# Performance work log

Hardware: AMD Instinct MI355X
Metric: run time of the kernel (lower is better)

The kernel has to match this reference:

```python
import jax, jax.numpy as jnp
import numpy as np
import math


def setup_inputs() -> dict:
    key = jax.random.key(0)
    k1, k2, k3 = jax.random.split(key, 3)
    shape = (2, 16, 2048, 64)  # (b, h, s, d)
    Q = jax.random.normal(k1, shape, dtype=jnp.float32)
    K = jax.random.normal(k2, shape, dtype=jnp.float32)
    V = jax.random.normal(k3, shape, dtype=jnp.float32)
    return {"Q": Q, "K": K, "V": V}


def reference(Q, K, V):
    b, h, s, d = Q.shape
    scale = jnp.float16(1.0 / math.sqrt(d))
    # Faithful to the torch module: fp16 QK^T and PV matmuls, fp32 softmax.
    Qh = Q.astype(jnp.float16)
    Kh = K.astype(jnp.float16)
    Vh = V.astype(jnp.float16)
    # [b,h,s,s] scores in fp16 (materialized, as in the original baddbmm)
    scores = jnp.einsum('bhsd,bhtd->bhst', Qh, Kh) * scale
    attn = jax.nn.softmax(scores.astype(jnp.float32), axis=-1).astype(jnp.float16)
    out = jnp.einsum('bhst,bhtd->bhsd', attn, Vh)
    return out.astype(jnp.float32)
```

## Files before the change

kernel.cpp:

```cpp
#include <hip/hip_runtime.h>
#include <stdint.h>

typedef _Float16 half8 __attribute__((ext_vector_type(8)));
typedef _Float16 half4 __attribute__((ext_vector_type(4)));
typedef __fp16 fp16x2 __attribute__((ext_vector_type(2)));
typedef float f32x4 __attribute__((ext_vector_type(4)));
typedef float float4v __attribute__((ext_vector_type(4)));

#define S_LEN 2048
#define D_DIM 64
#define QBLK 128
#define KVBLK 64
#define NT (S_LEN / KVBLK)
#define NBH 32
#define QSCALE 0.18033688f
#define KSTR 72

#if __has_builtin(__builtin_amdgcn_exp2f)
#define EXP2(x) __builtin_amdgcn_exp2f(x)
#else
#define EXP2(x) exp2f(x)
#endif
#define MAX3(a, b, c) fmaxf(fmaxf((a), (b)), (c))

static __device__ __forceinline__ void glds16(const void* g, void* l) {
  __builtin_amdgcn_global_load_lds(
      (__attribute__((address_space(1))) void*)(g),
      (__attribute__((address_space(3))) void*)(l), 16, 0, 0);
}
#define SBAR() do { asm volatile("" ::: "memory"); __builtin_amdgcn_s_barrier(); asm volatile("" ::: "memory"); } while (0)

__global__ __launch_bounds__(256)
void cvt_pack(const float* __restrict__ Kg, const float* __restrict__ Vg,
              _Float16* __restrict__ Kw, _Float16* __restrict__ Vw) {
  const int id = (int)(blockIdx.x * 256 + threadIdx.x);
  const int tensor = id >> 19;
  const int cid = id & 0x7FFFF;
  const int bht = cid >> 9;
  const int bh = bht >> 5, t = bht & 31;
  const int loc = cid & 511;
  const int a = loc >> 3;
  const int s = loc & 7;
  size_t srcoff;
  if (tensor == 0) {
    const int r = a;
    srcoff = (size_t)bh * (S_LEN * D_DIM) + (size_t)(t * 64 + r) * D_DIM + 8 * (s ^ (r & 7));
  } else {
    const int TI = a, c2 = s;
    const int it = TI & 3;
    const int vgi = ((TI >> 3) & 3) | (((TI >> 2) & 1) << 2) | (((TI >> 5) & 1) << 3);
    const int kq = c2 >> 1, d8 = (c2 & 1) * 8;
    srcoff = (size_t)bh * (S_LEN * D_DIM) + (size_t)(t * 64 + 4 * vgi + kq) * D_DIM + it * 16 + d8;
  }
  const float* src = (tensor ? Vg : Kg) + srcoff;
  float4v x = *(const float4v*)src;
  float4v y = *(const float4v*)(src + 4);
  half8 h = { (_Float16)x[0], (_Float16)x[1], (_Float16)x[2], (_Float16)x[3],
              (_Float16)y[0], (_Float16)y[1], (_Float16)y[2], (_Float16)y[3] };
  _Float16* dst = (tensor ? Vw : Kw) + (size_t)bht * 4096 + (size_t)loc * 8;
  *(half8*)dst = h;
}

static __device__ __forceinline__ void softmax_pack(f32x4 (&s)[4], float& m_run,
                                                    f32x4& l_acc, f32x4 (&o)[4],
                                                    half8 (&pb)[2]) {
  float plm;
  {
    float a0 = MAX3(s[0][0], s[0][1], s[0][2]);
    float a1 = MAX3(s[0][3], s[1][0], s[1][1]);
    float a2 = MAX3(s[1][2], s[1][3], s[2][0]);
    float a3 = MAX3(s[2][1], s[2][2], s[2][3]);
    float a4 = MAX3(s[3][0], s[3][1], s[3][2]);
    plm = fmaxf(MAX3(a0, a1, a2), MAX3(a3, a4, s[3][3]));
  }
  float p[16];
  if (__any(plm > m_run + 8.f)) {
    float pmax = fmaxf(plm, __shfl_xor(plm, 16, 64));
    pmax = fmaxf(pmax, __shfl_xor(pmax, 32, 64));
    const float mnew  = fmaxf(m_run, pmax);
    const float alpha = EXP2(m_run - mnew);
    m_run = mnew;
#pragma unroll
    for (int i = 0; i < 16; ++i)
      p[i] = EXP2(s[i >> 2][i & 3] - mnew);
    l_acc[0] *= alpha;
#pragma unroll
    for (int dt = 0; dt < 4; ++dt) {
      o[dt][0] *= alpha; o[dt][1] *= alpha;
      o[dt][2] *= alpha; o[dt][3] *= alpha;
    }
  } else {
#pragma unroll
    for (int i = 0; i < 16; ++i)
      p[i] = EXP2(s[i >> 2][i & 3] - m_run);
  }
#pragma unroll
  for (int kc = 0; kc < 2; ++kc) {
    fp16x2 x0 = __builtin_amdgcn_cvt_pkrtz(p[8 * kc + 0], p[8 * kc + 1]);
    fp16x2 x1 = __builtin_amdgcn_cvt_pkrtz(p[8 * kc + 2], p[8 * kc + 3]);
    fp16x2 x2 = __builtin_amdgcn_cvt_pkrtz(p[8 * kc + 4], p[8 * kc + 5]);
    fp16x2 x3 = __builtin_amdgcn_cvt_pkrtz(p[8 * kc + 6], p[8 * kc + 7]);
    half8 pk = { (_Float16)x0[0], (_Float16)x0[1], (_Float16)x1[0], (_Float16)x1[1],
                 (_Float16)x2[0], (_Float16)x2[1], (_Float16)x3[0], (_Float16)x3[1] };
    pb[kc] = pk;
  }
}

__global__ __launch_bounds__(256, 2)
void fa_fwd2(const float* __restrict__ Qg, const _Float16* __restrict__ Kw,
             const _Float16* __restrict__ Vw, float* __restrict__ Og) {
  __shared__ __attribute__((aligned(128))) _Float16 Klds[4][4096];
  __shared__ __attribute__((aligned(128))) _Float16 Vlds[4][4096];

  const int tid  = (int)threadIdx.x;
  const int wid  = tid >> 6;
  const int lane = tid & 63;
  const int g    = lane >> 4;
  const int c    = lane & 15;

  const int qtile = (int)blockIdx.x;
  const int bh    = (int)blockIdx.y;
  const size_t base = (size_t)bh * (S_LEN * D_DIM);

  const int qrowA = qtile * QBLK + wid * 16 + c;
  const int qrowB = qrowA + 64;
  half8 qfA[2], qfB[2];
#pragma unroll
  for (int kt = 0; kt < 2; ++kt) {
    const float* qpA = Qg + base + (size_t)qrowA * D_DIM + kt * 32 + 8 * g;
    const float* qpB = Qg + base + (size_t)qrowB * D_DIM + kt * 32 + 8 * g;
    float4v a0 = *(const float4v*)qpA;
    float4v a1 = *(const float4v*)(qpA + 4);
    float4v b0 = *(const float4v*)qpB;
    float4v b1 = *(const float4v*)(qpB + 4);
    half8 qa = { (_Float16)(a0[0] * QSCALE), (_Float16)(a0[1] * QSCALE),
                 (_Float16)(a0[2] * QSCALE), (_Float16)(a0[3] * QSCALE),
                 (_Float16)(a1[0] * QSCALE), (_Float16)(a1[1] * QSCALE),
                 (_Float16)(a1[2] * QSCALE), (_Float16)(a1[3] * QSCALE) };
    half8 qb = { (_Float16)(b0[0] * QSCALE), (_Float16)(b0[1] * QSCALE),
                 (_Float16)(b0[2] * QSCALE), (_Float16)(b0[3] * QSCALE),
                 (_Float16)(b1[0] * QSCALE), (_Float16)(b1[1] * QSCALE),
                 (_Float16)(b1[2] * QSCALE), (_Float16)(b1[3] * QSCALE) };
    qfA[kt] = qa; qfB[kt] = qb;
  }

  const f32x4 zero4 = {0.f, 0.f, 0.f, 0.f};
  f32x4 o_accA[4], o_accB[4];
#pragma unroll
  for (int i = 0; i < 4; ++i) { o_accA[i] = zero4; o_accB[i] = zero4; }
  f32x4 l_accA = zero4, l_accB = zero4;
  const half8 ones8 = { (_Float16)1.f, (_Float16)1.f, (_Float16)1.f, (_Float16)1.f,
                        (_Float16)1.f, (_Float16)1.f, (_Float16)1.f, (_Float16)1.f };
  float m_runA = -1.0e30f, m_runB = -1.0e30f;

  const char* kbase = (const char*)Kw + ((size_t)(bh * NT) << 13);
  const char* vbase = (const char*)Vw + ((size_t)(bh * NT) << 13);
  const int woff = wid * 2048 + lane * 16;

#define STAGE(b, t) do { \
    const char* ks_ = kbase + ((size_t)(t) << 13) + woff; \
    const char* vs_ = vbase + ((size_t)(t) << 13) + woff; \
    glds16(ks_,        &Klds[(b)][wid * 1024]); \
    glds16(ks_ + 1024, &Klds[(b)][wid * 1024 + 512]); \
    glds16(vs_,        &Vlds[(b)][wid * 1024]); \
    glds16(vs_ + 1024, &Vlds[(b)][wid * 1024 + 512]); \
  } while (0)

  const uint32_t vtb0 = (uint32_t)(uintptr_t)(&Vlds[0][0]) + 1024u * (uint32_t)g + 8u * (uint32_t)c;

  asm volatile("s_waitcnt vmcnt(0)" ::: "memory");
  STAGE(0, 0);
  STAGE(1, 1);

  for (int t = 0; t < NT; ++t) {
    if (t + 2 < NT) {
      STAGE((t + 2) & 3, t + 2);
      asm volatile("s_waitcnt vmcnt(8)" ::: "memory");
    } else if (t + 1 < NT) {
      asm volatile("s_waitcnt vmcnt(4)" ::: "memory");
    } else {
      asm volatile("s_waitcnt vmcnt(0)" ::: "memory");
    }
    __builtin_amdgcn_sched_barrier(0);
    SBAR();

    const _Float16* kcur = &Klds[t & 3][0];
    const uint32_t vt = vtb0 + (uint32_t)((t & 3) << 13);

    f32x4 sA[4], sB[4];
#pragma unroll
    for (int ct = 0; ct < 4; ++ct) { sA[ct] = zero4; sB[ct] = zero4; }
    __builtin_amdgcn_s_setprio(1);
#pragma unroll
    for (int ct = 0; ct < 4; ++ct) {
#pragma unroll
      for (int kt = 0; kt < 2; ++kt) {
        half8 kb = *(half8*)&kcur[(ct * 16 + c) * 64 + (((4 * kt + g) ^ (c & 7)) << 3)];
        sA[ct] = __builtin_amdgcn_mfma_f32_16x16x32_f16(kb, qfA[kt], sA[ct], 0, 0, 0);
        sB[ct] = __builtin_amdgcn_mfma_f32_16x16x32_f16(kb, qfB[kt], sB[ct], 0, 0, 0);
      }
    }
    __builtin_amdgcn_s_setprio(0);

    half4 vr[16];
#define TRRD(i, offstr) \
    asm volatile("ds_read_b64_tr_b16 %0, %1 offset:" offstr : "=v"(vr[i]) : "v"(vt))
    TRRD(0,  "0");    TRRD(1,  "128");  TRRD(2,  "256");  TRRD(3,  "384");
    TRRD(4,  "512");  TRRD(5,  "640");  TRRD(6,  "768");  TRRD(7,  "896");
    TRRD(8,  "4096"); TRRD(9,  "4224"); TRRD(10, "4352"); TRRD(11, "4480");
    TRRD(12, "4608"); TRRD(13, "4736"); TRRD(14, "4864"); TRRD(15, "4992");
#undef TRRD

    half8 pbA[2], pbB[2];
    softmax_pack(sA, m_runA, l_accA, o_accA, pbA);
    softmax_pack(sB, m_runB, l_accB, o_accB, pbB);

    asm volatile("s_waitcnt lgkmcnt(0)" ::: "memory");
    __builtin_amdgcn_sched_barrier(0);

    __builtin_amdgcn_s_setprio(1);
#pragma unroll
    for (int kc = 0; kc < 2; ++kc) {
#pragma unroll
      for (int dt = 0; dt < 4; ++dt) {
        half8 vf = __builtin_shufflevector(vr[kc * 8 + dt], vr[kc * 8 + 4 + dt],
                                           0, 1, 2, 3, 4, 5, 6, 7);
        o_accA[dt] = __builtin_amdgcn_mfma_f32_16x16x32_f16(vf, pbA[kc], o_accA[dt], 0, 0, 0);
        o_accB[dt] = __builtin_amdgcn_mfma_f32_16x16x32_f16(vf, pbB[kc], o_accB[dt], 0, 0, 0);
      }
      l_accA = __builtin_amdgcn_mfma_f32_16x16x32_f16(ones8, pbA[kc], l_accA, 0, 0, 0);
      l_accB = __builtin_amdgcn_mfma_f32_16x16x32_f16(ones8, pbB[kc], l_accB, 0, 0, 0);
    }
    __builtin_amdgcn_s_setprio(0);
  }
#undef STAGE

  const float invA = 1.0f / l_accA[0];
  const float invB = 1.0f / l_accB[0];
#pragma unroll
  for (int dt = 0; dt < 4; ++dt) {
    float4v wA = { o_accA[dt][0] * invA, o_accA[dt][1] * invA,
                   o_accA[dt][2] * invA, o_accA[dt][3] * invA };
    *(float4v*)&Og[base + (size_t)qrowA * D_DIM + dt * 16 + g * 4] = wA;
    float4v wB = { o_accB[dt][0] * invB, o_accB[dt][1] * invB,
                   o_accB[dt][2] * invB, o_accB[dt][3] * invB };
    *(float4v*)&Og[base + (size_t)qrowB * D_DIM + dt * 16 + g * 4] = wB;
  }
}

__global__ __launch_bounds__(256)
void fa_fwd_fb(const float* __restrict__ Qg, const float* __restrict__ Kg,
               const float* __restrict__ Vg, float* __restrict__ Og) {
  __shared__ _Float16 Klds[KVBLK * KSTR];
  __shared__ __attribute__((aligned(128))) _Float16 Vlds[KVBLK * D_DIM];

  const int tid  = (int)threadIdx.x;
  const int wid  = tid >> 6;
  const int lane = tid & 63;
  const int g    = lane >> 4;
  const int c    = lane & 15;

  const int qtile = (int)blockIdx.x;
  const int bh    = (int)blockIdx.y;
  const size_t base = (size_t)bh * (S_LEN * D_DIM);

  const int qrow = qtile * 64 + wid * 16 + c;
  half8 qf[2];
#pragma unroll
  for (int kt = 0; kt < 2; ++kt) {
    const float* qp = Qg + base + (size_t)qrow * D_DIM + kt * 32 + 8 * g;
    float4v a = *(const float4v*)qp;
    float4v b = *(const float4v*)(qp + 4);
    half8 q;
    q[0] = (_Float16)(a[0] * QSCALE); q[1] = (_Float16)(a[1] * QSCALE);
    q[2] = (_Float16)(a[2] * QSCALE); q[3] = (_Float16)(a[3] * QSCALE);
    q[4] = (_Float16)(b[0] * QSCALE); q[5] = (_Float16)(b[1] * QSCALE);
    q[6] = (_Float16)(b[2] * QSCALE); q[7] = (_Float16)(b[3] * QSCALE);
    qf[kt] = q;
  }

  const f32x4 zero4 = {0.f, 0.f, 0.f, 0.f};
  f32x4 o_acc[4];
#pragma unroll
  for (int i = 0; i < 4; ++i) o_acc[i] = zero4;
  float m_run = -1.0e30f, l_run = 0.f;

  const int srow = tid >> 4;
  const int scol = (tid & 15) * 4;
  const int vgi = tid >> 4;
  const int vlg = tid & 15;
  const int vk  = vgi * 4 + (vlg >> 2);
  const int vsub = 8 * (vgi & 3) + 4 * ((vgi >> 2) & 1) + 32 * (vgi >> 3);
  const uint32_t vtb = (uint32_t)(uintptr_t)(&Vlds[0]) + 1024u * (uint32_t)g + 8u * (uint32_t)c;

  for (int t = 0; t < NT; ++t) {
    const int kv0 = t * KVBLK;
    __syncthreads();
#pragma unroll
    for (int rr = 0; rr < 4; ++rr) {
      const int row = srow + rr * 16;
      const float* kp = Kg + base + (size_t)(kv0 + row) * D_DIM + scol;
      float4v kx = *(const float4v*)kp;
      half4 kh = { (_Float16)kx[0], (_Float16)kx[1], (_Float16)kx[2], (_Float16)kx[3] };
      *(half4*)&Klds[row * KSTR + scol] = kh;
    }
#pragma unroll
    for (int it = 0; it < 4; ++it) {
      const int d = it * 16 + (vlg & 3) * 4;
      const float* vp = Vg + base + (size_t)(kv0 + vk) * D_DIM + d;
      float4v vx = *(const float4v*)vp;
      half4 vh = { (_Float16)vx[0], (_Float16)vx[1], (_Float16)vx[2], (_Float16)vx[3] };
      *(half4*)&Vlds[(vsub + it) * 64 + (vlg >> 2) * 16 + (vlg & 3) * 4] = vh;
    }
    __syncthreads();

    f32x4 s_acc[4];
#pragma unroll
    for (int ct = 0; ct < 4; ++ct) s_acc[ct] = zero4;
#pragma unroll
    for (int ct = 0; ct < 4; ++ct) {
#pragma unroll
      for (int kt = 0; kt < 2; ++kt) {
        half8 kb = *(half8*)&Klds[(ct * 16 + c) * KSTR + kt * 32 + 8 * g];
        s_acc[ct] = __builtin_amdgcn_mfma_f32_16x16x32_f16(kb, qf[kt], s_acc[ct], 0, 0, 0);
      }
    }

    float pmax = -1.0e30f;
#pragma unroll
    for (int ct = 0; ct < 4; ++ct)
#pragma unroll
      for (int r = 0; r < 4; ++r) pmax = fmaxf(pmax, s_acc[ct][r]);
    pmax = fmaxf(pmax, __shfl_xor(pmax, 16, 64));
    pmax = fmaxf(pmax, __shfl_xor(pmax, 32, 64));
    const float mnew  = fmaxf(m_run, pmax);
    const float alpha = exp2f(m_run - mnew);
    m_run = mnew;

    float p[16];
    float psum = 0.f;
#pragma unroll
    for (int i = 0; i < 16; ++i) {
      p[i] = exp2f(s_acc[i >> 2][i & 3] - mnew);
      psum += p[i];
    }
    psum += __shfl_xor(psum, 16, 64);
    psum += __shfl_xor(psum, 32, 64);
    l_run = l_run * alpha + psum;
#pragma unroll
    for (int dt = 0; dt < 4; ++dt) {
      o_acc[dt][0] *= alpha; o_acc[dt][1] *= alpha;
      o_acc[dt][2] *= alpha; o_acc[dt][3] *= alpha;
    }

    half8 pb[2];
#pragma unroll
    for (int kc = 0; kc < 2; ++kc) {
      fp16x2 x0 = __builtin_amdgcn_cvt_pkrtz(p[8 * kc + 0], p[8 * kc + 1]);
      fp16x2 x1 = __builtin_amdgcn_cvt_pkrtz(p[8 * kc + 2], p[8 * kc + 3]);
      fp16x2 x2 = __builtin_amdgcn_cvt_pkrtz(p[8 * kc + 4], p[8 * kc + 5]);
      fp16x2 x3 = __builtin_amdgcn_cvt_pkrtz(p[8 * kc + 6], p[8 * kc + 7]);
      half8 pk = { (_Float16)x0[0], (_Float16)x0[1], (_Float16)x1[0], (_Float16)x1[1],
                   (_Float16)x2[0], (_Float16)x2[1], (_Float16)x3[0], (_Float16)x3[1] };
      pb[kc] = pk;
    }

    half4 vr[16];
#define TRRD(i, offstr) \
    asm volatile("ds_read_b64_tr_b16 %0, %1 offset:" offstr : "=v"(vr[i]) : "v"(vtb))
    TRRD(0,  "0");    TRRD(1,  "128");  TRRD(2,  "256");  TRRD(3,  "384");
    TRRD(4,  "512");  TRRD(5,  "640");  TRRD(6,  "768");  TRRD(7,  "896");
    TRRD(8,  "4096"); TRRD(9,  "4224"); TRRD(10, "4352"); TRRD(11, "4480");
    TRRD(12, "4608"); TRRD(13, "4736"); TRRD(14, "4864"); TRRD(15, "4992");
#undef TRRD
    asm volatile("s_waitcnt lgkmcnt(0)" ::: "memory");
    __builtin_amdgcn_sched_barrier(0);

#pragma unroll
    for (int kc = 0; kc < 2; ++kc) {
#pragma unroll
      for (int dt = 0; dt < 4; ++dt) {
        half8 vf = __builtin_shufflevector(vr[kc * 8 + dt], vr[kc * 8 + 4 + dt],
                                           0, 1, 2, 3, 4, 5, 6, 7);
        o_acc[dt] = __builtin_amdgcn_mfma_f32_16x16x32_f16(vf, pb[kc], o_acc[dt], 0, 0, 0);
      }
    }
  }

  const float invl = 1.0f / l_run;
#pragma unroll
  for (int dt = 0; dt < 4; ++dt) {
    float4v w = { o_acc[dt][0] * invl, o_acc[dt][1] * invl,
                  o_acc[dt][2] * invl, o_acc[dt][3] * invl };
    *(float4v*)&Og[base + (size_t)qrow * D_DIM + dt * 16 + g * 4] = w;
  }
}

extern "C" void kernel_launch(void* const* d_in, const int* in_sizes, int n_in,
                              void* d_out, int out_size, void* d_ws, size_t ws_size,
                              hipStream_t stream) {
  const float* Q = (const float*)d_in[0];
  const float* K = (const float*)d_in[1];
  const float* V = (const float*)d_in[2];
  float* O = (float*)d_out;
  dim3 block(256);
  if (ws_size >= (size_t)16 * 1024 * 1024) {
    _Float16* Kw = (_Float16*)d_ws;
    _Float16* Vw = Kw + (size_t)NBH * S_LEN * D_DIM;
    hipLaunchKernelGGL(cvt_pack, dim3(4096), block, 0, stream, K, V, Kw, Vw);
    hipLaunchKernelGGL(fa_fwd2, dim3(S_LEN / QBLK, NBH), block, 0, stream, Q, Kw, Vw, O);
  } else {
    hipLaunchKernelGGL(fa_fwd_fb, dim3(S_LEN / 64, NBH), block, 0, stream, Q, K, V, O);
  }
}
```

Measured before the change: 62.97 us.

## Use 16x16x16 MFMA for PV and deepen K/V prefetch to three tiles

Splits each P·V and row-sum MFMA into two 16x16x16 f16 MFMAs fed directly from the transposed LDS reads, avoiding the half8 shuffles. It also prefetches three KV tiles ahead, issued after the barrier into the buffer freed in the previous iteration. The split doubles the MFMA instruction count, and the x16 variant may have lower throughput than x32 on this chip.

```diff
diff --git a/kernel.cpp b/kernel.cpp
--- a/kernel.cpp
+++ b/kernel.cpp
@@ -22,6 +22,12 @@
 #define EXP2(x) exp2f(x)
 #endif
 #define MAX3(a, b, c) fmaxf(fmaxf((a), (b)), (c))
+
+#if __has_builtin(__builtin_amdgcn_mfma_f32_16x16x16f16)
+#define HAVE_MFMA16 1
+#else
+#define HAVE_MFMA16 0
+#endif
 
 static __device__ __forceinline__ void glds16(const void* g, void* l) {
   __builtin_amdgcn_global_load_lds(
@@ -61,9 +67,9 @@
   *(half8*)dst = h;
 }
 
-static __device__ __forceinline__ void softmax_pack(f32x4 (&s)[4], float& m_run,
-                                                    f32x4& l_acc, f32x4 (&o)[4],
-                                                    half8 (&pb)[2]) {
+static __device__ __forceinline__ void softmax_pack16(f32x4 (&s)[4], float& m_run,
+                                                      f32x4& l_acc, f32x4 (&o)[4],
+                                                      half4 (&pb)[2][2]) {
   float plm;
   {
     float a0 = MAX3(s[0][0], s[0][1], s[0][2]);
@@ -100,9 +106,10 @@
     fp16x2 x1 = __builtin_amdgcn_cvt_pkrtz(p[8 * kc + 2], p[8 * kc + 3]);
     fp16x2 x2 = __builtin_amdgcn_cvt_pkrtz(p[8 * kc + 4], p[8 * kc + 5]);
     fp16x2 x3 = __builtin_amdgcn_cvt_pkrtz(p[8 * kc + 6], p[8 * kc + 7]);
-    half8 pk = { (_Float16)x0[0], (_Float16)x0[1], (_Float16)x1[0], (_Float16)x1[1],
-                 (_Float16)x2[0], (_Float16)x2[1], (_Float16)x3[0], (_Float16)x3[1] };
-    pb[kc] = pk;
+    half4 lo = { (_Float16)x0[0], (_Float16)x0[1], (_Float16)x1[0], (_Float16)x1[1] };
+    half4 hi = { (_Float16)x2[0], (_Float16)x2[1], (_Float16)x3[0], (_Float16)x3[1] };
+    pb[kc][0] = lo;
+    pb[kc][1] = hi;
   }
 }
 
@@ -149,9 +156,13 @@
 #pragma unroll
   for (int i = 0; i < 4; ++i) { o_accA[i] = zero4; o_accB[i] = zero4; }
   f32x4 l_accA = zero4, l_accB = zero4;
+  float m_runA = -1.0e30f, m_runB = -1.0e30f;
+#if HAVE_MFMA16
+  const half4 ones4 = { (_Float16)1.f, (_Float16)1.f, (_Float16)1.f, (_Float16)1.f };
+#else
   const half8 ones8 = { (_Float16)1.f, (_Float16)1.f, (_Float16)1.f, (_Float16)1.f,
                         (_Float16)1.f, (_Float16)1.f, (_Float16)1.f, (_Float16)1.f };
-  float m_runA = -1.0e30f, m_runB = -1.0e30f;
+#endif
 
   const char* kbase = (const char*)Kw + ((size_t)(bh * NT) << 13);
   const char* vbase = (const char*)Vw + ((size_t)(bh * NT) << 13);
@@ -171,18 +182,19 @@
   asm volatile("s_waitcnt vmcnt(0)" ::: "memory");
   STAGE(0, 0);
   STAGE(1, 1);
+  STAGE(2, 2);
 
   for (int t = 0; t < NT; ++t) {
-    if (t + 2 < NT) {
-      STAGE((t + 2) & 3, t + 2);
+    if (t <= NT - 3) {
       asm volatile("s_waitcnt vmcnt(8)" ::: "memory");
-    } else if (t + 1 < NT) {
+    } else if (t == NT - 2) {
       asm volatile("s_waitcnt vmcnt(4)" ::: "memory");
     } else {
       asm volatile("s_waitcnt vmcnt(0)" ::: "memory");
     }
     __builtin_amdgcn_sched_barrier(0);
     SBAR();
+    if (t + 3 < NT) STAGE((t + 3) & 3, t + 3);
 
     const _Float16* kcur = &Klds[t & 3][0];
     const uint32_t vt = vtb0 + (uint32_t)((t & 3) << 13);
@@ -211,26 +223,46 @@
     TRRD(12, "4608"); TRRD(13, "4736"); TRRD(14, "4864"); TRRD(15, "4992");
 #undef TRRD
 
-    half8 pbA[2], pbB[2];
-    softmax_pack(sA, m_runA, l_accA, o_accA, pbA);
-    softmax_pack(sB, m_runB, l_accB, o_accB, pbB);
+    half4 pbA[2][2], pbB[2][2];
+    softmax_pack16(sA, m_runA, l_accA, o_accA, pbA);
+    softmax_pack16(sB, m_runB, l_accB, o_accB, pbB);
 
     asm volatile("s_waitcnt lgkmcnt(0)" ::: "memory");
     __builtin_amdgcn_sched_barrier(0);
 
     __builtin_amdgcn_s_setprio(1);
+#if HAVE_MFMA16
+#pragma unroll
+    for (int kc = 0; kc < 2; ++kc) {
+#pragma unroll
+      for (int h = 0; h < 2; ++h) {
+#pragma unroll
+        for (int dt = 0; dt < 4; ++dt) {
+          o_accA[dt] = __builtin_amdgcn_mfma_f32_16x16x16f16(vr[kc * 8 + h * 4 + dt], pbA[kc][h], o_accA[dt], 0, 0, 0);
+          o_accB[dt] = __builtin_amdgcn_mfma_f32_16x16x16f16(vr[kc * 8 + h * 4 + dt], pbB[kc][h], o_accB[dt], 0, 0, 0);
+        }
+        l_accA = __builtin_amdgcn_mfma_f32_16x16x16f16(ones4, pbA[kc][h], l_accA, 0, 0, 0);
+        l_accB = __builtin_amdgcn_mfma_f32_16x16x16f16(ones4, pbB[kc][h], l_accB, 0, 0, 0);
+      }
+    }
+#else
 #pragma unroll
     for (int kc = 0; kc < 2; ++kc) {
 #pragma unroll
       for (int dt = 0; dt < 4; ++dt) {
         half8 vf = __builtin_shufflevector(vr[kc * 8 + dt], vr[kc * 8 + 4 + dt],
                                            0, 1, 2, 3, 4, 5, 6, 7);
-        o_accA[dt] = __builtin_amdgcn_mfma_f32_16x16x32_f16(vf, pbA[kc], o_accA[dt], 0, 0, 0);
-        o_accB[dt] = __builtin_amdgcn_mfma_f32_16x16x32_f16(vf, pbB[kc], o_accB[dt], 0, 0, 0);
+        half8 pA = __builtin_shufflevector(pbA[kc][0], pbA[kc][1], 0, 1, 2, 3, 4, 5, 6, 7);
+        half8 pB = __builtin_shufflevector(pbB[kc][0], pbB[kc][1], 0, 1, 2, 3, 4, 5, 6, 7);
+        o_accA[dt] = __builtin_amdgcn_mfma_f32_16x16x32_f16(vf, pA, o_accA[dt], 0, 0, 0);
+        o_accB[dt] = __builtin_amdgcn_mfma_f32_16x16x32_f16(vf, pB, o_accB[dt], 0, 0, 0);
       }
-      l_accA = __builtin_amdgcn_mfma_f32_16x16x32_f16(ones8, pbA[kc], l_accA, 0, 0, 0);
-      l_accB = __builtin_amdgcn_mfma_f32_16x16x32_f16(ones8, pbB[kc], l_accB, 0, 0, 0);
-    }
+      half8 pA = __builtin_shufflevector(pbA[kc][0], pbA[kc][1], 0, 1, 2, 3, 4, 5, 6, 7);
+      half8 pB = __builtin_shufflevector(pbB[kc][0], pbB[kc][1], 0, 1, 2, 3, 4, 5, 6, 7);
+      l_accA = __builtin_amdgcn_mfma_f32_16x16x32_f16(ones8, pA, l_accA, 0, 0, 0);
+      l_accB = __builtin_amdgcn_mfma_f32_16x16x32_f16(ones8, pB, l_accB, 0, 0, 0);
+    }
+#endif
     __builtin_amdgcn_s_setprio(0);
   }
 #undef STAGE
```

New measurement: 70.37 us. +11.7%, slower.

## Software-pipeline PV matmul of previous tile with QK and softmax of current

Applied to the files above, without the earlier changes.

Restructures the attention main loop so the P·V MFMA block for tile t-1 runs after the QK^T MFMAs and V transpose-reads of tile t, and before tile t's softmax. Double-buffered V-fragment and P registers alternate across an unrolled-by-two loop, with a prologue and an epilogue PV. The goal is to hide LDS transpose-read latency and the softmax VALU work behind matrix-core work. The cost is extra live VGPRs for the second V and P buffers, which could lower occupancy or cause spills.

```diff
diff --git a/kernel.cpp b/kernel.cpp
--- a/kernel.cpp
+++ b/kernel.cpp
@@ -168,71 +168,98 @@
 
   const uint32_t vtb0 = (uint32_t)(uintptr_t)(&Vlds[0][0]) + 1024u * (uint32_t)g + 8u * (uint32_t)c;
 
+  half4 vr0[16], vr1[16];
+  half8 pbA0[2], pbB0[2], pbA1[2], pbB1[2];
+
+#define TRRD_SET(VR, vt) do { \
+    asm volatile("ds_read_b64_tr_b16 %0, %1 offset:0"    : "=v"(VR[0])  : "v"(vt)); \
+    asm volatile("ds_read_b64_tr_b16 %0, %1 offset:128"  : "=v"(VR[1])  : "v"(vt)); \
+    asm volatile("ds_read_b64_tr_b16 %0, %1 offset:256"  : "=v"(VR[2])  : "v"(vt)); \
+    asm volatile("ds_read_b64_tr_b16 %0, %1 offset:384"  : "=v"(VR[3])  : "v"(vt)); \
+    asm volatile("ds_read_b64_tr_b16 %0, %1 offset:512"  : "=v"(VR[4])  : "v"(vt)); \
+    asm volatile("ds_read_b64_tr_b16 %0, %1 offset:640"  : "=v"(VR[5])  : "v"(vt)); \
+    asm volatile("ds_read_b64_tr_b16 %0, %1 offset:768"  : "=v"(VR[6])  : "v"(vt)); \
+    asm volatile("ds_read_b64_tr_b16 %0, %1 offset:896"  : "=v"(VR[7])  : "v"(vt)); \
+    asm volatile("ds_read_b64_tr_b16 %0, %1 offset:4096" : "=v"(VR[8])  : "v"(vt)); \
+    asm volatile("ds_read_b64_tr_b16 %0, %1 offset:4224" : "=v"(VR[9])  : "v"(vt)); \
+    asm volatile("ds_read_b64_tr_b16 %0, %1 offset:4352" : "=v"(VR[10]) : "v"(vt)); \
+    asm volatile("ds_read_b64_tr_b16 %0, %1 offset:4480" : "=v"(VR[11]) : "v"(vt)); \
+    asm volatile("ds_read_b64_tr_b16 %0, %1 offset:4608" : "=v"(VR[12]) : "v"(vt)); \
+    asm volatile("ds_read_b64_tr_b16 %0, %1 offset:4736" : "=v"(VR[13]) : "v"(vt)); \
+    asm volatile("ds_read_b64_tr_b16 %0, %1 offset:4864" : "=v"(VR[14]) : "v"(vt)); \
+    asm volatile("ds_read_b64_tr_b16 %0, %1 offset:4992" : "=v"(VR[15]) : "v"(vt)); \
+  } while (0)
+
+#define PV_BLOCK(VR, PBA, PBB) do { \
+    __builtin_amdgcn_s_setprio(1); \
+    _Pragma("unroll") \
+    for (int kc = 0; kc < 2; ++kc) { \
+      _Pragma("unroll") \
+      for (int dt = 0; dt < 4; ++dt) { \
+        half8 vf = __builtin_shufflevector(VR[kc * 8 + dt], VR[kc * 8 + 4 + dt], \
+                                           0, 1, 2, 3, 4, 5, 6, 7); \
+        o_accA[dt] = __builtin_amdgcn_mfma_f32_16x16x32_f16(vf, PBA[kc], o_accA[dt], 0, 0, 0); \
+        o_accB[dt] = __builtin_amdgcn_mfma_f32_16x16x32_f16(vf, PBB[kc], o_accB[dt], 0, 0, 0); \
+      } \
+      l_accA = __builtin_amdgcn_mfma_f32_16x16x32_f16(ones8, PBA[kc], l_accA, 0, 0, 0); \
+      l_accB = __builtin_amdgcn_mfma_f32_16x16x32_f16(ones8, PBB[kc], l_accB, 0, 0, 0); \
+    } \
+    __builtin_amdgcn_s_setprio(0); \
+  } while (0)
+
+#define ITER(T, VRC, PBAC, PBBC, DO_PV, VRP, PBAP, PBBP) do { \
+    if ((T) + 2 < NT) { \
+      STAGE(((T) + 2) & 3, (T) + 2); \
+      asm volatile("s_waitcnt vmcnt(8)" ::: "memory"); \
+    } else if ((T) + 1 < NT) { \
+      asm volatile("s_waitcnt vmcnt(4)" ::: "memory"); \
+    } else { \
+      asm volatile("s_waitcnt vmcnt(0)" ::: "memory"); \
+    } \
+    __builtin_amdgcn_sched_barrier(0); \
+    SBAR(); \
+    const _Float16* kcur = &Klds[(T) & 3][0]; \
+    const uint32_t vt = vtb0 + (uint32_t)(((T) & 3) << 13); \
+    f32x4 sA[4], sB[4]; \
+    _Pragma("unroll") \
+    for (int ct = 0; ct < 4; ++ct) { sA[ct] = zero4; sB[ct] = zero4; } \
+    __builtin_amdgcn_s_setprio(1); \
+    _Pragma("unroll") \
+    for (int ct = 0; ct < 4; ++ct) { \
+      _Pragma("unroll") \
+      for (int kt = 0; kt < 2; ++kt) { \
+        half8 kb = *(half8*)&kcur[(ct * 16 + c) * 64 + (((4 * kt + g) ^ (c & 7)) << 3)]; \
+        sA[ct] = __builtin_amdgcn_mfma_f32_16x16x32_f16(kb, qfA[kt], sA[ct], 0, 0, 0); \
+        sB[ct] = __builtin_amdgcn_mfma_f32_16x16x32_f16(kb, qfB[kt], sB[ct], 0, 0, 0); \
+      } \
+    } \
+    __builtin_amdgcn_s_setprio(0); \
+    TRRD_SET(VRC, vt); \
+    if (DO_PV) { \
+      asm volatile("s_waitcnt lgkmcnt(15)" ::: "memory");  \
+      __builtin_amdgcn_sched_barrier(0); \
+      PV_BLOCK(VRP, PBAP, PBBP); \
+    } \
+    softmax_pack(sA, m_runA, l_accA, o_accA, PBAC); \
+    softmax_pack(sB, m_runB, l_accB, o_accB, PBBC); \
+  } while (0)
+
   asm volatile("s_waitcnt vmcnt(0)" ::: "memory");
   STAGE(0, 0);
   STAGE(1, 1);
 
-  for (int t = 0; t < NT; ++t) {
-    if (t + 2 < NT) {
-      STAGE((t + 2) & 3, t + 2);
-      asm volatile("s_waitcnt vmcnt(8)" ::: "memory");
-    } else if (t + 1 < NT) {
-      asm volatile("s_waitcnt vmcnt(4)" ::: "memory");
-    } else {
-      asm volatile("s_waitcnt vmcnt(0)" ::: "memory");
-    }
-    __builtin_amdgcn_sched_barrier(0);
-    SBAR();
-
-    const _Float16* kcur = &Klds[t & 3][0];
-    const uint32_t vt = vtb0 + (uint32_t)((t & 3) << 13);
-
-    f32x4 sA[4], sB[4];
-#pragma unroll
-    for (int ct = 0; ct < 4; ++ct) { sA[ct] = zero4; sB[ct] = zero4; }
-    __builtin_amdgcn_s_setprio(1);
-#pragma unroll
-    for (int ct = 0; ct < 4; ++ct) {
-#pragma unroll
-      for (int kt = 0; kt < 2; ++kt) {
-        half8 kb = *(half8*)&kcur[(ct * 16 + c) * 64 + (((4 * kt + g) ^ (c & 7)) << 3)];
-        sA[ct] = __builtin_amdgcn_mfma_f32_16x16x32_f16(kb, qfA[kt], sA[ct], 0, 0, 0);
-        sB[ct] = __builtin_amdgcn_mfma_f32_16x16x32_f16(kb, qfB[kt], sB[ct], 0, 0, 0);
-      }
-    }
-    __builtin_amdgcn_s_setprio(0);
-
-    half4 vr[16];
-#define TRRD(i, offstr) \
-    asm volatile("ds_read_b64_tr_b16 %0, %1 offset:" offstr : "=v"(vr[i]) : "v"(vt))
-    TRRD(0,  "0");    TRRD(1,  "128");  TRRD(2,  "256");  TRRD(3,  "384");
-    TRRD(4,  "512");  TRRD(5,  "640");  TRRD(6,  "768");  TRRD(7,  "896");
-    TRRD(8,  "4096"); TRRD(9,  "4224"); TRRD(10, "4352"); TRRD(11, "4480");
-    TRRD(12, "4608"); TRRD(13, "4736"); TRRD(14, "4864"); TRRD(15, "4992");
-#undef TRRD
-
-    half8 pbA[2], pbB[2];
-    softmax_pack(sA, m_runA, l_accA, o_accA, pbA);
-    softmax_pack(sB, m_runB, l_accB, o_accB, pbB);
-
-    asm volatile("s_waitcnt lgkmcnt(0)" ::: "memory");
-    __builtin_amdgcn_sched_barrier(0);
-
-    __builtin_amdgcn_s_setprio(1);
-#pragma unroll
-    for (int kc = 0; kc < 2; ++kc) {
-#pragma unroll
-      for (int dt = 0; dt < 4; ++dt) {
-        half8 vf = __builtin_shufflevector(vr[kc * 8 + dt], vr[kc * 8 + 4 + dt],
-                                           0, 1, 2, 3, 4, 5, 6, 7);
-        o_accA[dt] = __builtin_amdgcn_mfma_f32_16x16x32_f16(vf, pbA[kc], o_accA[dt], 0, 0, 0);
-        o_accB[dt] = __builtin_amdgcn_mfma_f32_16x16x32_f16(vf, pbB[kc], o_accB[dt], 0, 0, 0);
-      }
-      l_accA = __builtin_amdgcn_mfma_f32_16x16x32_f16(ones8, pbA[kc], l_accA, 0, 0, 0);
-      l_accB = __builtin_amdgcn_mfma_f32_16x16x32_f16(ones8, pbB[kc], l_accB, 0, 0, 0);
-    }
-    __builtin_amdgcn_s_setprio(0);
-  }
+  ITER(0, vr0, pbA0, pbB0, 0, vr1, pbA1, pbB1);
+  for (int t = 1; t + 1 < NT; t += 2) {
+    ITER(t,     vr1, pbA1, pbB1, 1, vr0, pbA0, pbB0);
+    ITER(t + 1, vr0, pbA0, pbB0, 1, vr1, pbA1, pbB1);
+  }
+  ITER(NT - 1, vr1, pbA1, pbB1, 1, vr0, pbA0, pbB0);
+  asm volatile("s_waitcnt lgkmcnt(0)" ::: "memory");
+  __builtin_amdgcn_sched_barrier(0);
+  PV_BLOCK(vr1, pbA1, pbB1);
+#undef ITER
+#undef PV_BLOCK
+#undef TRRD_SET
 #undef STAGE
 
   const float invA = 1.0f / l_accA[0];
```

Result: no change. 61.74 us (-2.0%).
